# Kernel optimization log

Hardware: AMD Instinct MI355X
Metric: run time of the kernel (lower is better)

The kernel has to match this reference:

```python
import jax, jax.numpy as jnp
import numpy as np

B, T, M, P = 512, 64, 256, 256


def setup_inputs() -> dict:
    key = jax.random.key(0)
    ks = jax.random.split(key, 17)
    w = lambda i, shape: (jax.random.normal(ks[i], shape, jnp.float32) * 0.05)
    return {
        "encoded_inputs": jax.random.normal(ks[0], (B, T, M), jnp.float32),
        "y": jax.random.normal(ks[1], (B, T, 1), jnp.float32),
        "tar": jax.random.normal(ks[2], (B, 2), jnp.float32),
        "train": 1,
        "Wd_w": w(3, (M, 2 * P)), "Wd_b": w(4, (M,)),
        "Ud_w": w(5, (M, M)),
        "vd_w": w(6, (1, M)),
        "wt_w": w(7, (1, M + 1)), "wt_b": w(8, (1,)),
        "Wy_w": w(9, (P, P + M)), "Wy_b": w(10, (P,)),
        "vy_w": w(11, (1, P)), "vy_b": w(12, (1,)),
        "Wih": w(13, (4 * P, 1)), "Whh": w(14, (4 * P, P)),
        "bih": w(15, (4 * P,)), "bhh": w(16, (4 * P,)),
    }


def _lstm_cell(x, h, c, Wih, Whh, bih, bhh):
    # torch.nn.LSTMCell gate order: i, f, g, o
    g = x @ Wih.T + h @ Whh.T + (bih + bhh)
    i, f, gg, o = jnp.split(g, 4, axis=1)
    c = jax.nn.sigmoid(f) * c + jax.nn.sigmoid(i) * jnp.tanh(gg)
    h = jax.nn.sigmoid(o) * jnp.tanh(c)
    return h, c


def reference(encoded_inputs, y, tar, train,
              Wd_w, Wd_b, Ud_w, vd_w, wt_w, wt_b,
              Wy_w, Wy_b, vy_w, vy_b, Wih, Whh, bih, bhh):
    Bn = encoded_inputs.shape[0]
    Pn = Whh.shape[1]
    Mn = encoded_inputs.shape[2]
    h0 = jnp.zeros((Bn, Pn), encoded_inputs.dtype)
    c0 = jnp.zeros((Bn, Pn), encoded_inputs.dtype)
    ctx0 = jnp.zeros((Bn, Mn), encoded_inputs.dtype)
    # U_d(encoded_inputs) is loop-invariant
    y1 = jnp.einsum('btm,nm->btn', encoded_inputs, Ud_w)  # (B,T,M)

    def attend(h, s):
        x1 = jnp.concatenate([h, s], axis=1) @ Wd_w.T + Wd_b      # (B,M)
        z1 = jnp.tanh(x1[:, None, :] + y1)                        # (B,T,M)
        l = jnp.einsum('btm,m->bt', z1, vd_w[0])                  # (B,T)
        beta = jax.nn.softmax(l, axis=1)
        return jnp.einsum('bt,btm->bm', beta, encoded_inputs)     # (B,M)

    def step(carry, y_t):
        h, s, _ = carry
        c_t = attend(h, s)
        y_til = jnp.concatenate([c_t, y_t], axis=1) @ wt_w.T + wt_b  # (B,1)
        h, s = _lstm_cell(y_til, h, s, Wih, Whh, bih, bhh)
        return (h, s, c_t), None

    (h, s, c_t), _ = jax.lax.scan(step, (h0, c0, ctx0), jnp.swapaxes(y, 0, 1))

    def head(h):
        return (jnp.concatenate([h, c_t], axis=1) @ Wy_w.T + Wy_b) @ vy_w.T + vy_b

    def extra(h, s, inp):
        y_til = jnp.concatenate([c_t, inp], axis=1) @ wt_w.T + wt_b
        h, s = _lstm_cell(y_til, h, s, Wih, Whh, bih, bhh)
        return h, s, head(h)

    y_Tp1 = head(h)
    if train:
        h, s, y_Tp2 = extra(h, s, tar[:, 0:1])
        h, s, y_Tp3 = extra(h, s, tar[:, 1:2])
    else:
        h, s, y_Tp2 = extra(h, s, y_Tp1)
        h, s, y_Tp3 = extra(h, s, y_Tp2)
    return (y_Tp1, y_Tp2, y_Tp3)
```

## Files before the change

### kernel.cpp

```cpp
#include <hip/hip_runtime.h>


typedef unsigned short u16;
typedef unsigned int u32;
typedef _Float16 half_t;
typedef half_t h2 __attribute__((ext_vector_type(2)));

#define BB 512
#define TT 64
#define MM 256
#define PP 256
#define YS 264
#define ES 68

#define WD16_OFF  0
#define WHH16_OFF 131072
#define WY16_OFF  393216
#define WQ_ELEMS  524288
#define WQ_BYTES  (WQ_ELEMS * 2)

struct H8 { h2 p[4]; };

#if defined(__has_builtin)
#if __has_builtin(__builtin_amdgcn_fdot2)
#define FDOT2(a, b, c) __builtin_amdgcn_fdot2((a), (b), (c), false)
#endif
#endif
#ifndef FDOT2
__device__ __forceinline__ float FDOT2(h2 a, h2 b, float c) {
  return c + (float)a[0] * (float)b[0] + (float)a[1] * (float)b[1];
}
#endif

__device__ __forceinline__ float dot8(const H8 w, const H8 a, float acc) {
  acc = FDOT2(w.p[0], a.p[0], acc);
  acc = FDOT2(w.p[1], a.p[1], acc);
  acc = FDOT2(w.p[2], a.p[2], acc);
  acc = FDOT2(w.p[3], a.p[3], acc);
  return acc;
}
__device__ __forceinline__ u16 f2h(float f) {
  union { half_t h; u16 u; } x; x.h = (half_t)f; return x.u;
}
__device__ __forceinline__ void unpackH8(const H8 v, float f[8]) {
#pragma unroll
  for (int i = 0; i < 8; ++i) f[i] = (float)v.p[i >> 1][i & 1];
}
__device__ __forceinline__ void ldf8(const float* p, float f[8]) {
  float4 a = *(const float4*)p;
  float4 b = *(const float4*)(p + 4);
  f[0]=a.x; f[1]=a.y; f[2]=a.z; f[3]=a.w;
  f[4]=b.x; f[5]=b.y; f[6]=b.z; f[7]=b.w;
}
__device__ __forceinline__ float tanh_fast(float x) {
  float e = __builtin_amdgcn_exp2f(x * 2.885390081777927f);
  return 1.0f - 2.0f * __builtin_amdgcn_rcpf(1.0f + e);
}
__device__ __forceinline__ float sigmoid_fast(float x) {
  float e = __builtin_amdgcn_exp2f(x * -1.4426950408889634f);
  return __builtin_amdgcn_rcpf(1.0f + e);
}

__global__ __launch_bounds__(256) void prep_kernel(
    const float* __restrict__ Wd, const float* __restrict__ Whh,
    const float* __restrict__ Wy, u16* __restrict__ o) {
  int i = blockIdx.x * 256 + threadIdx.x;
  float v;
  if (i < WHH16_OFF) {
    int ki = i & 7, n = (i >> 3) & 255, kb = i >> 11;
    v = Wd[n * 512 + kb * 8 + ki];
  } else if (i < WY16_OFF) {
    int r = i - WHH16_OFF;
    int ki = r & 7, n = (r >> 3) & 1023, kb = r >> 13;
    v = Whh[n * 256 + kb * 8 + ki];
  } else {
    int r = i - WY16_OFF;
    int ki = r & 7, n = (r >> 3) & 255, kb = r >> 11;
    v = Wy[n * 512 + kb * 8 + ki];
  }
  o[i] = f2h(v);
}

template <int WQ>
__global__ __launch_bounds__(256, 2) void scan_kernel(
    const float* __restrict__ E,
    const float* __restrict__ yin,
    const float* __restrict__ tar,
    const int*   __restrict__ train,
    const void*  __restrict__ Wd_q,
    const float* __restrict__ Wd_b,
    const float* __restrict__ Ud_w,
    const float* __restrict__ vd_w,
    const float* __restrict__ wt_w,
    const float* __restrict__ wt_b,
    const void*  __restrict__ Wy_q,
    const float* __restrict__ Wy_b,
    const float* __restrict__ vy_w,
    const float* __restrict__ vy_b,
    const float* __restrict__ Wih,
    const void*  __restrict__ Whh_q,
    const float* __restrict__ bih,
    const float* __restrict__ bhh,
    float* __restrict__ out)
{
  __shared__ __align__(16) u16   y1l[TT * YS];
  __shared__ __align__(16) u16   e16T[MM * ES];
  __shared__ __align__(16) u32   hs16[256];
  __shared__ __align__(16) u32   ctx16p[128];
  __shared__ __align__(16) float ctx[MM];
  __shared__ __align__(16) float x1s[MM];
  __shared__ __align__(16) float lpart[4][TT];
  __shared__ __align__(16) u16   betas16[TT];
  __shared__ float red[4];
  __shared__ float sc[2];

  const int j = threadIdx.x;
  const int b = blockIdx.x;
  const int wv = j >> 6;

  hs16[j] = 0;
  float creg = 0.f;

  {
    const float* __restrict__ Eb = E + (size_t)b * TT * MM;
    for (int i = j; i < TT * MM; i += 256) {
      int t = i >> 8, m = i & 255;
      e16T[m * ES + t] = f2h(Eb[i]);
    }
  }

  {
    const float* __restrict__ Eb = E + (size_t)b * TT * MM;
    const float* __restrict__ Uj = Ud_w + (size_t)j * MM;
    for (int t0 = 0; t0 < TT; t0 += 16) {
      float acc[16];
#pragma unroll
      for (int i = 0; i < 16; ++i) acc[i] = 0.f;
      for (int m0 = 0; m0 < MM; m0 += 8) {
        float w[8]; ldf8(Uj + m0, w);
#pragma unroll
        for (int tt = 0; tt < 16; ++tt) {
          float e[8]; ldf8(Eb + (size_t)(t0 + tt) * MM + m0, e);
#pragma unroll
          for (int mm = 0; mm < 8; ++mm) acc[tt] = fmaf(e[mm], w[mm], acc[tt]);
        }
      }
#pragma unroll
      for (int tt = 0; tt < 16; ++tt)
        y1l[(t0 + tt) * YS + j] = f2h(acc[tt]);
    }
  }
  __syncthreads();

  auto mv4 = [&](float& g0, float& g1, float& g2, float& g3) {
    g0 = g1 = g2 = g3 = 0.f;
    if (WQ) {
      const u16* W = (const u16*)Whh_q;
      const u16* p0 = W + (size_t)j * 8;
      const u16* p1 = p0 + 256 * 8;
      const u16* p2 = p0 + 512 * 8;
      const u16* p3 = p0 + 768 * 8;
#pragma unroll 4
      for (int kb = 0; kb < 32; ++kb) {
        H8 hp = *(const H8*)&hs16[kb * 4];
        g0 = dot8(*(const H8*)p0, hp, g0); p0 += 8192;
        g1 = dot8(*(const H8*)p1, hp, g1); p1 += 8192;
        g2 = dot8(*(const H8*)p2, hp, g2); p2 += 8192;
        g3 = dot8(*(const H8*)p3, hp, g3); p3 += 8192;
      }
    } else {
      const float* W = (const float*)Whh_q;
      const float* p0 = W + (size_t)j * 256;
#pragma unroll 2
      for (int kb = 0; kb < 32; ++kb) {
        H8 hp = *(const H8*)&hs16[kb * 4];
        float hf[8]; unpackH8(hp, hf);
        float w0[8], w1[8], w2[8], w3[8];
        ldf8(p0 + kb * 8, w0);
        ldf8(p0 + 256 * 256 + kb * 8, w1);
        ldf8(p0 + 512 * 256 + kb * 8, w2);
        ldf8(p0 + 768 * 256 + kb * 8, w3);
#pragma unroll
        for (int i = 0; i < 8; ++i) {
          g0 = fmaf(hf[i], w0[i], g0);
          g1 = fmaf(hf[i], w1[i], g1);
          g2 = fmaf(hf[i], w2[i], g2);
          g3 = fmaf(hf[i], w3[i], g3);
        }
      }
    }
  };

  auto gates_apply = [&](float g0, float g1, float g2, float g3, float ytil) {
    g0 += ytil * Wih[j]       + bih[j]       + bhh[j];
    g1 += ytil * Wih[j + 256] + bih[j + 256] + bhh[j + 256];
    g2 += ytil * Wih[j + 512] + bih[j + 512] + bhh[j + 512];
    g3 += ytil * Wih[j + 768] + bih[j + 768] + bhh[j + 768];
    float c = sigmoid_fast(g1) * creg + sigmoid_fast(g0) * tanh_fast(g2);
    float h = sigmoid_fast(g3) * tanh_fast(c);
    creg = c;
    u16* hsu = (u16*)hs16;
    hsu[j] = f2h(h);
    hsu[256 + j] = f2h(c);
  };

  auto head_store = [&](int outIdx) {
    float p = 0.f;
    if (WQ) {
      const u16* W = (const u16*)Wy_q;
      const u16* ph = W + (size_t)j * 8;
      const u16* pc = W + (size_t)(32 * 256 + j) * 8;
#pragma unroll 4
      for (int kb = 0; kb < 32; ++kb) {
        H8 hp = *(const H8*)&hs16[kb * 4];
        H8 cp = *(const H8*)&ctx16p[kb * 4];
        p = dot8(*(const H8*)ph, hp, p); ph += 2048;
        p = dot8(*(const H8*)pc, cp, p); pc += 2048;
      }
    } else {
      const float* W = (const float*)Wy_q + (size_t)j * 512;
      for (int kb = 0; kb < 32; ++kb) {
        H8 hp = *(const H8*)&hs16[kb * 4];
        float hf[8]; unpackH8(hp, hf);
        float w0[8], w1[8];
        ldf8(W + kb * 8, w0);
        ldf8(W + 256 + kb * 8, w1);
#pragma unroll
        for (int i = 0; i < 8; ++i) {
          p = fmaf(hf[i], w0[i], p);
          p = fmaf(ctx[kb * 8 + i], w1[i], p);
        }
      }
    }
    float pp = (p + Wy_b[j]) * vy_w[j];
#pragma unroll
    for (int off = 32; off; off >>= 1) pp += __shfl_xor(pp, off, 64);
    if ((j & 63) == 0) red[wv] = pp;
    __syncthreads();
    if (j == 0) {
      float o = red[0] + red[1] + red[2] + red[3] + vy_b[0];
      out[(size_t)outIdx * BB + b] = o;
      sc[0] = o;
    }
    __syncthreads();
  };

  for (int step = 0; step < TT; ++step) {
    float ax0 = 0.f, ax1 = 0.f, g0, g1, g2, g3;
    {
      if (WQ) {
        const u16* Wd16 = (const u16*)Wd_q;
        const u16* Wh16 = (const u16*)Whh_q;
        const u16* pdh = Wd16 + (size_t)j * 8;
        const u16* pdc = Wd16 + (size_t)(32 * 256 + j) * 8;
        const u16* p0 = Wh16 + (size_t)j * 8;
        const u16* p1 = p0 + 256 * 8;
        const u16* p2 = p0 + 512 * 8;
        const u16* p3 = p0 + 768 * 8;
        float b0 = 0.f, b1 = 0.f, b2 = 0.f, b3 = 0.f;
#pragma unroll 4
        for (int kb = 0; kb < 32; ++kb) {
          H8 hp = *(const H8*)&hs16[kb * 4];
          H8 cp = *(const H8*)&hs16[128 + kb * 4];
          ax0 = dot8(*(const H8*)pdh, hp, ax0); pdh += 2048;
          ax1 = dot8(*(const H8*)pdc, cp, ax1); pdc += 2048;
          b0 = dot8(*(const H8*)p0, hp, b0); p0 += 8192;
          b1 = dot8(*(const H8*)p1, hp, b1); p1 += 8192;
          b2 = dot8(*(const H8*)p2, hp, b2); p2 += 8192;
          b3 = dot8(*(const H8*)p3, hp, b3); p3 += 8192;
        }
        g0 = b0; g1 = b1; g2 = b2; g3 = b3;
      } else {
        const float* wd = (const float*)Wd_q + (size_t)j * 512;
        const float* w0p = (const float*)Whh_q + (size_t)j * 256;
        float b0 = 0.f, b1 = 0.f, b2 = 0.f, b3 = 0.f;
#pragma unroll 2
        for (int kb = 0; kb < 32; ++kb) {
          H8 hp = *(const H8*)&hs16[kb * 4];
          H8 cp = *(const H8*)&hs16[128 + kb * 4];
          float hf[8], cf[8]; unpackH8(hp, hf); unpackH8(cp, cf);
          float wh[8], wc[8], w0[8], w1[8], w2[8], w3[8];
          ldf8(wd + kb * 8, wh);
          ldf8(wd + 256 + kb * 8, wc);
          ldf8(w0p + kb * 8, w0);
          ldf8(w0p + 256 * 256 + kb * 8, w1);
          ldf8(w0p + 512 * 256 + kb * 8, w2);
          ldf8(w0p + 768 * 256 + kb * 8, w3);
#pragma unroll
          for (int i = 0; i < 8; ++i) {
            ax0 = fmaf(hf[i], wh[i], ax0);
            ax1 = fmaf(cf[i], wc[i], ax1);
            b0 = fmaf(hf[i], w0[i], b0);
            b1 = fmaf(hf[i], w1[i], b1);
            b2 = fmaf(hf[i], w2[i], b2);
            b3 = fmaf(hf[i], w3[i], b3);
          }
        }
        g0 = b0; g1 = b1; g2 = b2; g3 = b3;
      }
      x1s[j] = ax0 + ax1 + Wd_b[j];
    }
    __syncthreads();

    {
      const int q = wv, tq = j & 63;
      const u16* __restrict__ yrow = &y1l[tq * YS + q * 64];
      const float* __restrict__ xp = &x1s[q * 64];
      const float* __restrict__ vp = vd_w + q * 64;
      float lp = 0.f;
#pragma unroll 2
      for (int m0 = 0; m0 < 64; m0 += 8) {
        H8 yv = *(const H8*)(yrow + m0);
        float yf[8]; unpackH8(yv, yf);
        float xf[8]; ldf8(xp + m0, xf);
        float vf[8]; ldf8(vp + m0, vf);
#pragma unroll
        for (int mm = 0; mm < 8; ++mm) {
          float z = tanh_fast(xf[mm] + yf[mm]);
          lp = fmaf(z, vf[mm], lp);
        }
      }
      lpart[q][tq] = lp;
    }
    __syncthreads();

    if (j < 64) {
      const int t = j;
      float l = lpart[0][t] + lpart[1][t] + lpart[2][t] + lpart[3][t];
      float mx = l;
#pragma unroll
      for (int off = 32; off; off >>= 1) mx = fmaxf(mx, __shfl_xor(mx, off, 64));
      float e = __builtin_amdgcn_exp2f((l - mx) * 1.4426950408889634f);
      float sm = e;
#pragma unroll
      for (int off = 32; off; off >>= 1) sm += __shfl_xor(sm, off, 64);
      betas16[t] = f2h(e * __builtin_amdgcn_rcpf(sm));
    }
    __syncthreads();

    {
      const u16* __restrict__ ep = &e16T[j * ES];
      float acc = 0.f;
#pragma unroll
      for (int t0 = 0; t0 < TT; t0 += 8) {
        h2 e0 = *(const h2*)(ep + t0);
        h2 e1 = *(const h2*)(ep + t0 + 2);
        h2 e2 = *(const h2*)(ep + t0 + 4);
        h2 e3 = *(const h2*)(ep + t0 + 6);
        H8 bp = *(const H8*)&betas16[t0];
        acc = FDOT2(bp.p[0], e0, acc);
        acc = FDOT2(bp.p[1], e1, acc);
        acc = FDOT2(bp.p[2], e2, acc);
        acc = FDOT2(bp.p[3], e3, acc);
      }
      ctx[j] = acc;
      ((u16*)ctx16p)[j] = f2h(acc);
    }
    {
      float p = ctx[j] * wt_w[j];
#pragma unroll
      for (int off = 32; off; off >>= 1) p += __shfl_xor(p, off, 64);
      if ((j & 63) == 0) red[wv] = p;
    }
    __syncthreads();
    {
      float ytil = red[0] + red[1] + red[2] + red[3]
                 + yin[(size_t)b * TT + step] * wt_w[MM] + wt_b[0];
      gates_apply(g0, g1, g2, g3, ytil);
    }
    __syncthreads();
  }

  float ctdot;
  {
    float p = ctx[j] * wt_w[j];
#pragma unroll
    for (int off = 32; off; off >>= 1) p += __shfl_xor(p, off, 64);
    if ((j & 63) == 0) red[wv] = p;
    __syncthreads();
    ctdot = red[0] + red[1] + red[2] + red[3];
    __syncthreads();
  }

  head_store(0);

  const int tr = train[0];
  for (int e = 0; e < 2; ++e) {
    float inp = tr ? tar[(size_t)b * 2 + e] : sc[0];
    float ytil = ctdot + inp * wt_w[MM] + wt_b[0];
    float g0, g1, g2, g3;
    mv4(g0, g1, g2, g3);
    gates_apply(g0, g1, g2, g3, ytil);
    __syncthreads();
    head_store(1 + e);
  }
}

extern "C" void kernel_launch(void* const* d_in, const int* in_sizes, int n_in,
                              void* d_out, int out_size, void* d_ws, size_t ws_size,
                              hipStream_t stream) {
  const float* E     = (const float*)d_in[0];
  const float* yin   = (const float*)d_in[1];
  const float* tar   = (const float*)d_in[2];
  const int*   train = (const int*)d_in[3];
  const float* Wd_w  = (const float*)d_in[4];
  const float* Wd_b  = (const float*)d_in[5];
  const float* Ud_w  = (const float*)d_in[6];
  const float* vd_w  = (const float*)d_in[7];
  const float* wt_w  = (const float*)d_in[8];
  const float* wt_b  = (const float*)d_in[9];
  const float* Wy_w  = (const float*)d_in[10];
  const float* Wy_b  = (const float*)d_in[11];
  const float* vy_w  = (const float*)d_in[12];
  const float* vy_b  = (const float*)d_in[13];
  const float* Wih   = (const float*)d_in[14];
  const float* Whh   = (const float*)d_in[15];
  const float* bih   = (const float*)d_in[16];
  const float* bhh   = (const float*)d_in[17];

  float* out = (float*)d_out;

  if (ws_size >= (size_t)WQ_BYTES) {
    u16* wq = (u16*)d_ws;
    prep_kernel<<<dim3(WQ_ELEMS / 256), dim3(256), 0, stream>>>(
        Wd_w, Whh, Wy_w, wq);
    scan_kernel<1><<<dim3(BB), dim3(256), 0, stream>>>(
        E, yin, tar, train, wq + WD16_OFF, Wd_b, Ud_w, vd_w, wt_w, wt_b,
        wq + WY16_OFF, Wy_b, vy_w, vy_b, Wih, wq + WHH16_OFF, bih, bhh, out);
  } else {
    scan_kernel<0><<<dim3(BB), dim3(256), 0, stream>>>(
        E, yin, tar, train, Wd_w, Wd_b, Ud_w, vd_w, wt_w, wt_b,
        Wy_w, Wy_b, vy_w, vy_b, Wih, Whh, bih, bhh, out);
  }

  (void)in_sizes; (void)n_in; (void)out_size;
}
```

Measured before the change: 1.189 ms.

## Process two batch rows per block to share weight loads across rows

Each 512-thread block now handles two batch elements. Every Whh/Wd/Wy weight row is loaded once and applied to both rows' hidden states, which roughly halves global weight traffic per batch element. The transposed LDS copy of E is removed: E is converted to fp16 in a separate prep kernel and the context sum reads it from global memory using beta values broadcast by shuffle. This adds extra barriers and cross-half partial-sum exchanges through LDS, doubles per-block LDS, and adds per-step global reads of E.

```diff
diff --git a/kernel.cpp b/kernel.cpp
--- a/kernel.cpp
+++ b/kernel.cpp
@@ -11,13 +11,15 @@
 #define MM 256
 #define PP 256
 #define YS 264
-#define ES 68
 
 #define WD16_OFF  0
 #define WHH16_OFF 131072
 #define WY16_OFF  393216
 #define WQ_ELEMS  524288
-#define WQ_BYTES  (WQ_ELEMS * 2)
+#define E16_OFF   524288
+#define E16_ELEMS (BB * TT * MM)
+#define WS_ELEMS  (WQ_ELEMS + E16_ELEMS)
+#define WS_BYTES  (WS_ELEMS * 2)
 
 struct H8 { h2 p[4]; };
 
@@ -61,7 +63,7 @@
   return __builtin_amdgcn_rcpf(1.0f + e);
 }
 
-__global__ __launch_bounds__(256) void prep_kernel(
+__global__ __launch_bounds__(256) void prep_w(
     const float* __restrict__ Wd, const float* __restrict__ Whh,
     const float* __restrict__ Wy, u16* __restrict__ o) {
   int i = blockIdx.x * 256 + threadIdx.x;
@@ -81,8 +83,14 @@
   o[i] = f2h(v);
 }
 
+__global__ __launch_bounds__(256) void prep_e(
+    const float* __restrict__ E, u16* __restrict__ o) {
+  int i = blockIdx.x * 256 + threadIdx.x;
+  o[E16_OFF + i] = f2h(E[i]);
+}
+
 template <int WQ>
-__global__ __launch_bounds__(256, 2) void scan_kernel(
+__global__ __launch_bounds__(512, 2) void scan_kernel(
     const float* __restrict__ E,
     const float* __restrict__ yin,
     const float* __restrict__ tar,
@@ -101,33 +109,29 @@
     const void*  __restrict__ Whh_q,
     const float* __restrict__ bih,
     const float* __restrict__ bhh,
+    const u16*   __restrict__ E16,
     float* __restrict__ out)
 {
-  __shared__ __align__(16) u16   y1l[TT * YS];
-  __shared__ __align__(16) u16   e16T[MM * ES];
-  __shared__ __align__(16) u32   hs16[256];
-  __shared__ __align__(16) u32   ctx16p[128];
-  __shared__ __align__(16) float ctx[MM];
-  __shared__ __align__(16) float x1s[MM];
-  __shared__ __align__(16) float lpart[4][TT];
-  __shared__ __align__(16) u16   betas16[TT];
-  __shared__ float red[4];
-  __shared__ float sc[2];
-
-  const int j = threadIdx.x;
-  const int b = blockIdx.x;
-  const int wv = j >> 6;
-
-  hs16[j] = 0;
+  __shared__ __align__(16) u16   y1l[2][TT * YS];
+  __shared__ __align__(16) u32   hs16[2 * 256];
+  __shared__ __align__(16) u32   ctx16p[2 * 128];
+  __shared__ __align__(16) float gbuf[2][1024];
+  __shared__ __align__(16) float part[2][2][256];
+  __shared__ __align__(16) float x1s[2][MM];
+  __shared__ __align__(16) float ctx[2][MM];
+  __shared__ __align__(16) float lpart[2][4][TT];
+  __shared__ float red[2][4];
+  __shared__ float sc_head[2];
+
+  const int tid  = threadIdx.x;
+  const int half = tid >> 8;
+  const int j    = tid & 255;
+  const int wv   = (tid >> 6) & 3;
+  const int lane = tid & 63;
+  const int b    = blockIdx.x * 2 + half;
+
+  hs16[tid] = 0;
   float creg = 0.f;
-
-  {
-    const float* __restrict__ Eb = E + (size_t)b * TT * MM;
-    for (int i = j; i < TT * MM; i += 256) {
-      int t = i >> 8, m = i & 255;
-      e16T[m * ES + t] = f2h(Eb[i]);
-    }
-  }
 
   {
     const float* __restrict__ Eb = E + (size_t)b * TT * MM;
@@ -147,166 +151,184 @@
       }
 #pragma unroll
       for (int tt = 0; tt < 16; ++tt)
-        y1l[(t0 + tt) * YS + j] = f2h(acc[tt]);
+        y1l[half][(t0 + tt) * YS + j] = f2h(acc[tt]);
     }
   }
   __syncthreads();
 
-  auto mv4 = [&](float& g0, float& g1, float& g2, float& g3) {
-    g0 = g1 = g2 = g3 = 0.f;
+  auto whh_mv = [&]() {
+    float b00 = 0.f, b01 = 0.f, b10 = 0.f, b11 = 0.f;
     if (WQ) {
-      const u16* W = (const u16*)Whh_q;
-      const u16* p0 = W + (size_t)j * 8;
-      const u16* p1 = p0 + 256 * 8;
-      const u16* p2 = p0 + 512 * 8;
-      const u16* p3 = p0 + 768 * 8;
+      const u16* p1 = (const u16*)Whh_q + (size_t)tid * 8;
+      const u16* p2 = p1 + 512 * 8;
 #pragma unroll 4
       for (int kb = 0; kb < 32; ++kb) {
-        H8 hp = *(const H8*)&hs16[kb * 4];
-        g0 = dot8(*(const H8*)p0, hp, g0); p0 += 8192;
-        g1 = dot8(*(const H8*)p1, hp, g1); p1 += 8192;
-        g2 = dot8(*(const H8*)p2, hp, g2); p2 += 8192;
-        g3 = dot8(*(const H8*)p3, hp, g3); p3 += 8192;
+        H8 h0 = *(const H8*)&hs16[kb * 4];
+        H8 h1 = *(const H8*)&hs16[256 + kb * 4];
+        H8 w1 = *(const H8*)p1; p1 += 8192;
+        H8 w2 = *(const H8*)p2; p2 += 8192;
+        b00 = dot8(w1, h0, b00);
+        b01 = dot8(w1, h1, b01);
+        b10 = dot8(w2, h0, b10);
+        b11 = dot8(w2, h1, b11);
       }
     } else {
-      const float* W = (const float*)Whh_q;
-      const float* p0 = W + (size_t)j * 256;
+      const float* q1 = (const float*)Whh_q + (size_t)tid * 256;
+      const float* q2 = q1 + 512 * 256;
 #pragma unroll 2
       for (int kb = 0; kb < 32; ++kb) {
-        H8 hp = *(const H8*)&hs16[kb * 4];
-        float hf[8]; unpackH8(hp, hf);
-        float w0[8], w1[8], w2[8], w3[8];
-        ldf8(p0 + kb * 8, w0);
-        ldf8(p0 + 256 * 256 + kb * 8, w1);
-        ldf8(p0 + 512 * 256 + kb * 8, w2);
-        ldf8(p0 + 768 * 256 + kb * 8, w3);
+        H8 h0 = *(const H8*)&hs16[kb * 4];
+        H8 h1 = *(const H8*)&hs16[256 + kb * 4];
+        float f0[8], f1[8]; unpackH8(h0, f0); unpackH8(h1, f1);
+        float w1[8], w2[8];
+        ldf8(q1 + kb * 8, w1);
+        ldf8(q2 + kb * 8, w2);
 #pragma unroll
         for (int i = 0; i < 8; ++i) {
-          g0 = fmaf(hf[i], w0[i], g0);
-          g1 = fmaf(hf[i], w1[i], g1);
-          g2 = fmaf(hf[i], w2[i], g2);
-          g3 = fmaf(hf[i], w3[i], g3);
-        }
-      }
-    }
+          b00 = fmaf(f0[i], w1[i], b00);
+          b01 = fmaf(f1[i], w1[i], b01);
+          b10 = fmaf(f0[i], w2[i], b10);
+          b11 = fmaf(f1[i], w2[i], b11);
+        }
+      }
+    }
+    gbuf[0][tid] = b00;       gbuf[1][tid] = b01;
+    gbuf[0][tid + 512] = b10; gbuf[1][tid + 512] = b11;
   };
 
-  auto gates_apply = [&](float g0, float g1, float g2, float g3, float ytil) {
-    g0 += ytil * Wih[j]       + bih[j]       + bhh[j];
-    g1 += ytil * Wih[j + 256] + bih[j + 256] + bhh[j + 256];
-    g2 += ytil * Wih[j + 512] + bih[j + 512] + bhh[j + 512];
-    g3 += ytil * Wih[j + 768] + bih[j + 768] + bhh[j + 768];
+  auto gates_apply = [&](float ytil) {
+    float g0 = gbuf[half][j]       + ytil * Wih[j]       + bih[j]       + bhh[j];
+    float g1 = gbuf[half][j + 256] + ytil * Wih[j + 256] + bih[j + 256] + bhh[j + 256];
+    float g2 = gbuf[half][j + 512] + ytil * Wih[j + 512] + bih[j + 512] + bhh[j + 512];
+    float g3 = gbuf[half][j + 768] + ytil * Wih[j + 768] + bih[j + 768] + bhh[j + 768];
     float c = sigmoid_fast(g1) * creg + sigmoid_fast(g0) * tanh_fast(g2);
     float h = sigmoid_fast(g3) * tanh_fast(c);
     creg = c;
     u16* hsu = (u16*)hs16;
-    hsu[j] = f2h(h);
-    hsu[256 + j] = f2h(c);
+    hsu[half * 512 + j]       = f2h(h);
+    hsu[half * 512 + 256 + j] = f2h(c);
   };
 
   auto head_store = [&](int outIdx) {
-    float p = 0.f;
+    float p0 = 0.f, p1 = 0.f;
     if (WQ) {
-      const u16* W = (const u16*)Wy_q;
-      const u16* ph = W + (size_t)j * 8;
-      const u16* pc = W + (size_t)(32 * 256 + j) * 8;
+      const u16* pw = (const u16*)Wy_q + (size_t)half * 32 * 2048 + (size_t)j * 8;
+      const u32* a0 = half ? &ctx16p[0] : &hs16[0];
+      const u32* a1 = half ? &ctx16p[128] : &hs16[256];
 #pragma unroll 4
       for (int kb = 0; kb < 32; ++kb) {
-        H8 hp = *(const H8*)&hs16[kb * 4];
-        H8 cp = *(const H8*)&ctx16p[kb * 4];
-        p = dot8(*(const H8*)ph, hp, p); ph += 2048;
-        p = dot8(*(const H8*)pc, cp, p); pc += 2048;
+        H8 w = *(const H8*)pw; pw += 2048;
+        p0 = dot8(w, *(const H8*)&a0[kb * 4], p0);
+        p1 = dot8(w, *(const H8*)&a1[kb * 4], p1);
       }
     } else {
-      const float* W = (const float*)Wy_q + (size_t)j * 512;
+      const float* pw = (const float*)Wy_q + (size_t)j * 512 + half * 256;
       for (int kb = 0; kb < 32; ++kb) {
-        H8 hp = *(const H8*)&hs16[kb * 4];
-        float hf[8]; unpackH8(hp, hf);
-        float w0[8], w1[8];
-        ldf8(W + kb * 8, w0);
-        ldf8(W + 256 + kb * 8, w1);
-#pragma unroll
-        for (int i = 0; i < 8; ++i) {
-          p = fmaf(hf[i], w0[i], p);
-          p = fmaf(ctx[kb * 8 + i], w1[i], p);
-        }
-      }
-    }
-    float pp = (p + Wy_b[j]) * vy_w[j];
-#pragma unroll
-    for (int off = 32; off; off >>= 1) pp += __shfl_xor(pp, off, 64);
-    if ((j & 63) == 0) red[wv] = pp;
+        float w[8]; ldf8(pw + kb * 8, w);
+        if (half) {
+#pragma unroll
+          for (int i = 0; i < 8; ++i) {
+            p0 = fmaf(ctx[0][kb * 8 + i], w[i], p0);
+            p1 = fmaf(ctx[1][kb * 8 + i], w[i], p1);
+          }
+        } else {
+          H8 h0 = *(const H8*)&hs16[kb * 4];
+          H8 h1 = *(const H8*)&hs16[256 + kb * 4];
+          float f0[8], f1[8]; unpackH8(h0, f0); unpackH8(h1, f1);
+#pragma unroll
+          for (int i = 0; i < 8; ++i) {
+            p0 = fmaf(f0[i], w[i], p0);
+            p1 = fmaf(f1[i], w[i], p1);
+          }
+        }
+      }
+    }
+    part[half][0][j] = p0;
+    part[half][1][j] = p1;
+    __syncthreads();
+    {
+      float hp = part[0][half][j] + part[1][half][j] + Wy_b[j];
+      float pp = hp * vy_w[j];
+#pragma unroll
+      for (int off = 32; off; off >>= 1) pp += __shfl_xor(pp, off, 64);
+      if (lane == 0) red[half][wv] = pp;
+    }
     __syncthreads();
     if (j == 0) {
-      float o = red[0] + red[1] + red[2] + red[3] + vy_b[0];
+      float o = red[half][0] + red[half][1] + red[half][2] + red[half][3]
+              + vy_b[0];
       out[(size_t)outIdx * BB + b] = o;
-      sc[0] = o;
+      sc_head[half] = o;
     }
     __syncthreads();
   };
 
   for (int step = 0; step < TT; ++step) {
-    float ax0 = 0.f, ax1 = 0.f, g0, g1, g2, g3;
     {
+      float ax0 = 0.f, ax1 = 0.f;
+      float b00 = 0.f, b01 = 0.f, b10 = 0.f, b11 = 0.f;
       if (WQ) {
-        const u16* Wd16 = (const u16*)Wd_q;
-        const u16* Wh16 = (const u16*)Whh_q;
-        const u16* pdh = Wd16 + (size_t)j * 8;
-        const u16* pdc = Wd16 + (size_t)(32 * 256 + j) * 8;
-        const u16* p0 = Wh16 + (size_t)j * 8;
-        const u16* p1 = p0 + 256 * 8;
-        const u16* p2 = p0 + 512 * 8;
-        const u16* p3 = p0 + 768 * 8;
-        float b0 = 0.f, b1 = 0.f, b2 = 0.f, b3 = 0.f;
+        const u16* pd = (const u16*)Wd_q + (size_t)half * 32 * 2048 + (size_t)j * 8;
+        const u16* p1 = (const u16*)Whh_q + (size_t)tid * 8;
+        const u16* p2 = p1 + 512 * 8;
+        const int ao = half * 128;
 #pragma unroll 4
         for (int kb = 0; kb < 32; ++kb) {
-          H8 hp = *(const H8*)&hs16[kb * 4];
-          H8 cp = *(const H8*)&hs16[128 + kb * 4];
-          ax0 = dot8(*(const H8*)pdh, hp, ax0); pdh += 2048;
-          ax1 = dot8(*(const H8*)pdc, cp, ax1); pdc += 2048;
-          b0 = dot8(*(const H8*)p0, hp, b0); p0 += 8192;
-          b1 = dot8(*(const H8*)p1, hp, b1); p1 += 8192;
-          b2 = dot8(*(const H8*)p2, hp, b2); p2 += 8192;
-          b3 = dot8(*(const H8*)p3, hp, b3); p3 += 8192;
-        }
-        g0 = b0; g1 = b1; g2 = b2; g3 = b3;
+          H8 h0 = *(const H8*)&hs16[kb * 4];
+          H8 h1 = *(const H8*)&hs16[256 + kb * 4];
+          H8 a0 = *(const H8*)&hs16[ao + kb * 4];
+          H8 a1 = *(const H8*)&hs16[256 + ao + kb * 4];
+          H8 wd = *(const H8*)pd; pd += 2048;
+          H8 w1 = *(const H8*)p1; p1 += 8192;
+          H8 w2 = *(const H8*)p2; p2 += 8192;
+          ax0 = dot8(wd, a0, ax0);
+          ax1 = dot8(wd, a1, ax1);
+          b00 = dot8(w1, h0, b00);
+          b01 = dot8(w1, h1, b01);
+          b10 = dot8(w2, h0, b10);
+          b11 = dot8(w2, h1, b11);
+        }
       } else {
-        const float* wd = (const float*)Wd_q + (size_t)j * 512;
-        const float* w0p = (const float*)Whh_q + (size_t)j * 256;
-        float b0 = 0.f, b1 = 0.f, b2 = 0.f, b3 = 0.f;
+        const float* pd = (const float*)Wd_q + (size_t)j * 512 + half * 256;
+        const float* q1 = (const float*)Whh_q + (size_t)tid * 256;
+        const float* q2 = q1 + 512 * 256;
+        const int ao = half * 128;
 #pragma unroll 2
         for (int kb = 0; kb < 32; ++kb) {
-          H8 hp = *(const H8*)&hs16[kb * 4];
-          H8 cp = *(const H8*)&hs16[128 + kb * 4];
-          float hf[8], cf[8]; unpackH8(hp, hf); unpackH8(cp, cf);
-          float wh[8], wc[8], w0[8], w1[8], w2[8], w3[8];
-          ldf8(wd + kb * 8, wh);
-          ldf8(wd + 256 + kb * 8, wc);
-          ldf8(w0p + kb * 8, w0);
-          ldf8(w0p + 256 * 256 + kb * 8, w1);
-          ldf8(w0p + 512 * 256 + kb * 8, w2);
-          ldf8(w0p + 768 * 256 + kb * 8, w3);
+          H8 h0 = *(const H8*)&hs16[kb * 4];
+          H8 h1 = *(const H8*)&hs16[256 + kb * 4];
+          H8 c0 = *(const H8*)&hs16[ao + kb * 4];
+          H8 c1 = *(const H8*)&hs16[256 + ao + kb * 4];
+          float f0[8], f1[8], e0[8], e1[8];
+          unpackH8(h0, f0); unpackH8(h1, f1); unpackH8(c0, e0); unpackH8(c1, e1);
+          float wd[8], w1[8], w2[8];
+          ldf8(pd + kb * 8, wd);
+          ldf8(q1 + kb * 8, w1);
+          ldf8(q2 + kb * 8, w2);
 #pragma unroll
           for (int i = 0; i < 8; ++i) {
-            ax0 = fmaf(hf[i], wh[i], ax0);
-            ax1 = fmaf(cf[i], wc[i], ax1);
-            b0 = fmaf(hf[i], w0[i], b0);
-            b1 = fmaf(hf[i], w1[i], b1);
-            b2 = fmaf(hf[i], w2[i], b2);
-            b3 = fmaf(hf[i], w3[i], b3);
+            ax0 = fmaf(e0[i], wd[i], ax0);
+            ax1 = fmaf(e1[i], wd[i], ax1);
+            b00 = fmaf(f0[i], w1[i], b00);
+            b01 = fmaf(f1[i], w1[i], b01);
+            b10 = fmaf(f0[i], w2[i], b10);
+            b11 = fmaf(f1[i], w2[i], b11);
           }
         }
-        g0 = b0; g1 = b1; g2 = b2; g3 = b3;
-      }
-      x1s[j] = ax0 + ax1 + Wd_b[j];
-    }
+      }
+      part[half][0][j] = ax0;
+      part[half][1][j] = ax1;
+      gbuf[0][tid] = b00;       gbuf[1][tid] = b01;
+      gbuf[0][tid + 512] = b10; gbuf[1][tid + 512] = b11;
+    }
+    __syncthreads();
+    x1s[half][j] = part[0][half][j] + part[1][half][j] + Wd_b[j];
     __syncthreads();
 
     {
-      const int q = wv, tq = j & 63;
-      const u16* __restrict__ yrow = &y1l[tq * YS + q * 64];
-      const float* __restrict__ xp = &x1s[q * 64];
-      const float* __restrict__ vp = vd_w + q * 64;
+      const u16* __restrict__ yrow = &y1l[half][lane * YS + wv * 64];
+      const float* __restrict__ xp = &x1s[half][wv * 64];
+      const float* __restrict__ vp = vd_w + wv * 64;
       float lp = 0.f;
 #pragma unroll 2
       for (int m0 = 0; m0 < 64; m0 += 8) {
@@ -320,13 +342,14 @@
           lp = fmaf(z, vf[mm], lp);
         }
       }
-      lpart[q][tq] = lp;
-    }
-    __syncthreads();
-
-    if (j < 64) {
-      const int t = j;
-      float l = lpart[0][t] + lpart[1][t] + lpart[2][t] + lpart[3][t];
+      lpart[half][wv][lane] = lp;
+    }
+    __syncthreads();
+
+    float ctv;
+    {
+      float l = lpart[half][0][lane] + lpart[half][1][lane]
+              + lpart[half][2][lane] + lpart[half][3][lane];
       float mx = l;
 #pragma unroll
       for (int off = 32; off; off >>= 1) mx = fmaxf(mx, __shfl_xor(mx, off, 64));
@@ -334,63 +357,62 @@
       float sm = e;
 #pragma unroll
       for (int off = 32; off; off >>= 1) sm += __shfl_xor(sm, off, 64);
-      betas16[t] = f2h(e * __builtin_amdgcn_rcpf(sm));
+      float beta = e * __builtin_amdgcn_rcpf(sm);
+
+      float acc = 0.f;
+      if (WQ) {
+        const half_t* __restrict__ ep = (const half_t*)E16 + (size_t)b * TT * MM + j;
+#pragma unroll 8
+        for (int t = 0; t < TT; ++t) {
+          float bt = __shfl(beta, t, 64);
+          acc = fmaf(bt, (float)ep[(size_t)t * MM], acc);
+        }
+      } else {
+        const float* __restrict__ ep = E + (size_t)b * TT * MM + j;
+#pragma unroll 8
+        for (int t = 0; t < TT; ++t) {
+          float bt = __shfl(beta, t, 64);
+          acc = fmaf(bt, ep[(size_t)t * MM], acc);
+        }
+      }
+      ctv = acc;
+      ctx[half][j] = acc;
+      ((u16*)ctx16p)[half * 256 + j] = f2h(acc);
+
+      float p = ctv * wt_w[j];
+#pragma unroll
+      for (int off = 32; off; off >>= 1) p += __shfl_xor(p, off, 64);
+      if (lane == 0) red[half][wv] = p;
     }
     __syncthreads();
 
     {
-      const u16* __restrict__ ep = &e16T[j * ES];
-      float acc = 0.f;
-#pragma unroll
-      for (int t0 = 0; t0 < TT; t0 += 8) {
-        h2 e0 = *(const h2*)(ep + t0);
-        h2 e1 = *(const h2*)(ep + t0 + 2);
-        h2 e2 = *(const h2*)(ep + t0 + 4);
-        h2 e3 = *(const h2*)(ep + t0 + 6);
-        H8 bp = *(const H8*)&betas16[t0];
-        acc = FDOT2(bp.p[0], e0, acc);
-        acc = FDOT2(bp.p[1], e1, acc);
-        acc = FDOT2(bp.p[2], e2, acc);
-        acc = FDOT2(bp.p[3], e3, acc);
-      }
-      ctx[j] = acc;
-      ((u16*)ctx16p)[j] = f2h(acc);
-    }
-    {
-      float p = ctx[j] * wt_w[j];
-#pragma unroll
-      for (int off = 32; off; off >>= 1) p += __shfl_xor(p, off, 64);
-      if ((j & 63) == 0) red[wv] = p;
-    }
-    __syncthreads();
-    {
-      float ytil = red[0] + red[1] + red[2] + red[3]
+      float ytil = red[half][0] + red[half][1] + red[half][2] + red[half][3]
                  + yin[(size_t)b * TT + step] * wt_w[MM] + wt_b[0];
-      gates_apply(g0, g1, g2, g3, ytil);
+      gates_apply(ytil);
     }
     __syncthreads();
   }
 
   float ctdot;
   {
-    float p = ctx[j] * wt_w[j];
+    float p = ctx[half][j] * wt_w[j];
 #pragma unroll
     for (int off = 32; off; off >>= 1) p += __shfl_xor(p, off, 64);
-    if ((j & 63) == 0) red[wv] = p;
-    __syncthreads();
-    ctdot = red[0] + red[1] + red[2] + red[3];
-    __syncthreads();
+    if (lane == 0) red[half][wv] = p;
+    __syncthreads();
+    ctdot = red[half][0] + red[half][1] + red[half][2] + red[half][3];
   }
 
   head_store(0);
 
   const int tr = train[0];
   for (int e = 0; e < 2; ++e) {
-    float inp = tr ? tar[(size_t)b * 2 + e] : sc[0];
+    float inp = tr ? tar[(size_t)b * 2 + e] : sc_head[half];
     float ytil = ctdot + inp * wt_w[MM] + wt_b[0];
-    float g0, g1, g2, g3;
-    mv4(g0, g1, g2, g3);
-    gates_apply(g0, g1, g2, g3, ytil);
+    whh_mv();
+    __syncthreads();
+    gates_apply(ytil);
     __syncthreads();
     head_store(1 + e);
   }
@@ -420,17 +442,18 @@
 
   float* out = (float*)d_out;
 
-  if (ws_size >= (size_t)WQ_BYTES) {
+  if (ws_size >= (size_t)WS_BYTES) {
     u16* wq = (u16*)d_ws;
-    prep_kernel<<<dim3(WQ_ELEMS / 256), dim3(256), 0, stream>>>(
-        Wd_w, Whh, Wy_w, wq);
-    scan_kernel<1><<<dim3(BB), dim3(256), 0, stream>>>(
+    prep_w<<<dim3(WQ_ELEMS / 256), dim3(256), 0, stream>>>(Wd_w, Whh, Wy_w, wq);
+    prep_e<<<dim3(E16_ELEMS / 256), dim3(256), 0, stream>>>(E, wq);
+    scan_kernel<1><<<dim3(BB / 2), dim3(512), 0, stream>>>(
         E, yin, tar, train, wq + WD16_OFF, Wd_b, Ud_w, vd_w, wt_w, wt_b,
-        wq + WY16_OFF, Wy_b, vy_w, vy_b, Wih, wq + WHH16_OFF, bih, bhh, out);
+        wq + WY16_OFF, Wy_b, vy_w, vy_b, Wih, wq + WHH16_OFF, bih, bhh,
+        wq + E16_OFF, out);
   } else {
-    scan_kernel<0><<<dim3(BB), dim3(256), 0, stream>>>(
+    scan_kernel<0><<<dim3(BB / 2), dim3(512), 0, stream>>>(
         E, yin, tar, train, Wd_w, Wd_b, Ud_w, vd_w, wt_w, wt_b,
-        Wy_w, Wy_b, vy_w, vy_b, Wih, Whh, bih, bhh, out);
+        Wy_w, Wy_b, vy_w, vy_b, Wih, Whh, bih, bhh, (const u16*)nullptr, out);
   }
 
   (void)in_sizes; (void)n_in; (void)out_size;
```

Result: no change. 1.195 ms (+0.5%).

## Compute softmax and context per wavefront redundantly to eliminate block barriers

Applied to the files above, without the earlier changes.

Each wavefront now computes the full softmax over time and the full context vector itself, using a private copy of the attention weights. The wt dot product is reduced within a wave, so the cross-wave reduction is gone. The barrier after the x1 write is dropped because each wave reads only the x1 entries it wrote. Together these cut the block-wide synchronisations per timestep from five to two. In exchange, the context computation is repeated four times, once per wave.

```diff
diff --git a/kernel.cpp b/kernel.cpp
--- a/kernel.cpp
+++ b/kernel.cpp
@@ -17,7 +17,7 @@
 #define WHH16_OFF 131072
 #define WY16_OFF  393216
 #define WQ_ELEMS  524288
-#define WQ_BYTES  (WQ_ELEMS * 2)
+#define WQ_BYTES  ((size_t)WQ_ELEMS * 2)
 
 struct H8 { h2 p[4]; };
 
@@ -61,7 +61,7 @@
   return __builtin_amdgcn_rcpf(1.0f + e);
 }
 
-__global__ __launch_bounds__(256) void prep_kernel(
+__global__ __launch_bounds__(256) void prep_w(
     const float* __restrict__ Wd, const float* __restrict__ Whh,
     const float* __restrict__ Wy, u16* __restrict__ o) {
   int i = blockIdx.x * 256 + threadIdx.x;
@@ -110,13 +110,14 @@
   __shared__ __align__(16) float ctx[MM];
   __shared__ __align__(16) float x1s[MM];
   __shared__ __align__(16) float lpart[4][TT];
-  __shared__ __align__(16) u16   betas16[TT];
-  __shared__ float red[4];
-  __shared__ float sc[2];
-
-  const int j = threadIdx.x;
-  const int b = blockIdx.x;
-  const int wv = j >> 6;
+  __shared__ __align__(16) u16   betas_w[4 * TT];
+  __shared__ float red[4], red2[4];
+  __shared__ float sc_head[1];
+
+  const int j    = threadIdx.x;
+  const int b    = blockIdx.x;
+  const int wv   = j >> 6;
+  const int lane = j & 63;
 
   hs16[j] = 0;
   float creg = 0.f;
@@ -152,11 +153,10 @@
   }
   __syncthreads();
 
-  auto mv4 = [&](float& g0, float& g1, float& g2, float& g3) {
+  auto whh_mv = [&](float& g0, float& g1, float& g2, float& g3) {
     g0 = g1 = g2 = g3 = 0.f;
     if (WQ) {
-      const u16* W = (const u16*)Whh_q;
-      const u16* p0 = W + (size_t)j * 8;
+      const u16* p0 = (const u16*)Whh_q + (size_t)j * 8;
       const u16* p1 = p0 + 256 * 8;
       const u16* p2 = p0 + 512 * 8;
       const u16* p3 = p0 + 768 * 8;
@@ -169,8 +169,7 @@
         g3 = dot8(*(const H8*)p3, hp, g3); p3 += 8192;
       }
     } else {
-      const float* W = (const float*)Whh_q;
-      const float* p0 = W + (size_t)j * 256;
+      const float* p0 = (const float*)Whh_q + (size_t)j * 256;
 #pragma unroll 2
       for (int kb = 0; kb < 32; ++kb) {
         H8 hp = *(const H8*)&hs16[kb * 4];
@@ -200,16 +199,15 @@
     float h = sigmoid_fast(g3) * tanh_fast(c);
     creg = c;
     u16* hsu = (u16*)hs16;
-    hsu[j] = f2h(h);
+    hsu[j]       = f2h(h);
     hsu[256 + j] = f2h(c);
   };
 
   auto head_store = [&](int outIdx) {
     float p = 0.f;
     if (WQ) {
-      const u16* W = (const u16*)Wy_q;
-      const u16* ph = W + (size_t)j * 8;
-      const u16* pc = W + (size_t)(32 * 256 + j) * 8;
+      const u16* ph = (const u16*)Wy_q + (size_t)j * 8;
+      const u16* pc = (const u16*)Wy_q + (size_t)(32 * 256 + j) * 8;
 #pragma unroll 4
       for (int kb = 0; kb < 32; ++kb) {
         H8 hp = *(const H8*)&hs16[kb * 4];
@@ -235,25 +233,24 @@
     float pp = (p + Wy_b[j]) * vy_w[j];
 #pragma unroll
     for (int off = 32; off; off >>= 1) pp += __shfl_xor(pp, off, 64);
-    if ((j & 63) == 0) red[wv] = pp;
+    if (lane == 0) red[wv] = pp;
     __syncthreads();
     if (j == 0) {
       float o = red[0] + red[1] + red[2] + red[3] + vy_b[0];
       out[(size_t)outIdx * BB + b] = o;
-      sc[0] = o;
+      sc_head[0] = o;
     }
     __syncthreads();
   };
 
   for (int step = 0; step < TT; ++step) {
-    float ax0 = 0.f, ax1 = 0.f, g0, g1, g2, g3;
+    float g0, g1, g2, g3;
     {
+      float ax0 = 0.f, ax1 = 0.f;
       if (WQ) {
-        const u16* Wd16 = (const u16*)Wd_q;
-        const u16* Wh16 = (const u16*)Whh_q;
-        const u16* pdh = Wd16 + (size_t)j * 8;
-        const u16* pdc = Wd16 + (size_t)(32 * 256 + j) * 8;
-        const u16* p0 = Wh16 + (size_t)j * 8;
+        const u16* pdh = (const u16*)Wd_q + (size_t)j * 8;
+        const u16* pdc = (const u16*)Wd_q + (size_t)(32 * 256 + j) * 8;
+        const u16* p0 = (const u16*)Whh_q + (size_t)j * 8;
         const u16* p1 = p0 + 256 * 8;
         const u16* p2 = p0 + 512 * 8;
         const u16* p3 = p0 + 768 * 8;
@@ -300,13 +297,11 @@
       }
       x1s[j] = ax0 + ax1 + Wd_b[j];
     }
-    __syncthreads();
 
     {
-      const int q = wv, tq = j & 63;
-      const u16* __restrict__ yrow = &y1l[tq * YS + q * 64];
-      const float* __restrict__ xp = &x1s[q * 64];
-      const float* __restrict__ vp = vd_w + q * 64;
+      const u16* __restrict__ yrow = &y1l[lane * YS + wv * 64];
+      const float* __restrict__ xp = &x1s[wv * 64];
+      const float* __restrict__ vp = vd_w + wv * 64;
       float lp = 0.f;
 #pragma unroll 2
       for (int m0 = 0; m0 < 64; m0 += 8) {
@@ -320,13 +315,13 @@
           lp = fmaf(z, vf[mm], lp);
         }
       }
-      lpart[q][tq] = lp;
-    }
-    __syncthreads();
-
-    if (j < 64) {
-      const int t = j;
-      float l = lpart[0][t] + lpart[1][t] + lpart[2][t] + lpart[3][t];
+      lpart[wv][lane] = lp;
+    }
+    __syncthreads();
+
+    {
+      float l = lpart[0][lane] + lpart[1][lane]
+              + lpart[2][lane] + lpart[3][lane];
       float mx = l;
 #pragma unroll
       for (int off = 32; off; off >>= 1) mx = fmaxf(mx, __shfl_xor(mx, off, 64));
@@ -334,38 +329,31 @@
       float sm = e;
 #pragma unroll
       for (int off = 32; off; off >>= 1) sm += __shfl_xor(sm, off, 64);
-      betas16[t] = f2h(e * __builtin_amdgcn_rcpf(sm));
-    }
-    __syncthreads();
-
-    {
-      const u16* __restrict__ ep = &e16T[j * ES];
-      float acc = 0.f;
-#pragma unroll
-      for (int t0 = 0; t0 < TT; t0 += 8) {
-        h2 e0 = *(const h2*)(ep + t0);
-        h2 e1 = *(const h2*)(ep + t0 + 2);
-        h2 e2 = *(const h2*)(ep + t0 + 4);
-        h2 e3 = *(const h2*)(ep + t0 + 6);
-        H8 bp = *(const H8*)&betas16[t0];
-        acc = FDOT2(bp.p[0], e0, acc);
-        acc = FDOT2(bp.p[1], e1, acc);
-        acc = FDOT2(bp.p[2], e2, acc);
-        acc = FDOT2(bp.p[3], e3, acc);
-      }
-      ctx[j] = acc;
-      ((u16*)ctx16p)[j] = f2h(acc);
-    }
-    {
-      float p = ctx[j] * wt_w[j];
+      float beta = e * __builtin_amdgcn_rcpf(sm);
+      betas_w[wv * 64 + lane] = f2h(beta);
+
+      float ct[4];
+#pragma unroll
+      for (int q = 0; q < 4; ++q) {
+        const u16* __restrict__ ep = &e16T[(q * 64 + lane) * ES];
+        float acc = 0.f;
+#pragma unroll
+        for (int t0 = 0; t0 < TT; t0 += 8) {
+          H8 bp = *(const H8*)&betas_w[wv * 64 + t0];
+          H8 ev = *(const H8*)(ep + t0);
+          acc = dot8(bp, ev, acc);
+        }
+        ct[q] = acc;
+      }
+      ctx[wv * 64 + lane] = ct[wv];
+      ((u16*)ctx16p)[wv * 64 + lane] = f2h(ct[wv]);
+
+      float p = ct[0] * wt_w[lane]       + ct[1] * wt_w[64 + lane]
+              + ct[2] * wt_w[128 + lane] + ct[3] * wt_w[192 + lane];
 #pragma unroll
       for (int off = 32; off; off >>= 1) p += __shfl_xor(p, off, 64);
-      if ((j & 63) == 0) red[wv] = p;
-    }
-    __syncthreads();
-    {
-      float ytil = red[0] + red[1] + red[2] + red[3]
-                 + yin[(size_t)b * TT + step] * wt_w[MM] + wt_b[0];
+      float ytil = p + yin[(size_t)b * TT + step] * wt_w[MM] + wt_b[0];
+
       gates_apply(g0, g1, g2, g3, ytil);
     }
     __syncthreads();
@@ -376,9 +364,9 @@
     float p = ctx[j] * wt_w[j];
 #pragma unroll
     for (int off = 32; off; off >>= 1) p += __shfl_xor(p, off, 64);
-    if ((j & 63) == 0) red[wv] = p;
-    __syncthreads();
-    ctdot = red[0] + red[1] + red[2] + red[3];
+    if (lane == 0) red2[wv] = p;
+    __syncthreads();
+    ctdot = red2[0] + red2[1] + red2[2] + red2[3];
     __syncthreads();
   }
 
@@ -386,10 +374,11 @@
 
   const int tr = train[0];
   for (int e = 0; e < 2; ++e) {
-    float inp = tr ? tar[(size_t)b * 2 + e] : sc[0];
+    float g0, g1, g2, g3;
+    whh_mv(g0, g1, g2, g3);
+    __syncthreads();
+    float inp = tr ? tar[(size_t)b * 2 + e] : sc_head[0];
     float ytil = ctdot + inp * wt_w[MM] + wt_b[0];
-    float g0, g1, g2, g3;
-    mv4(g0, g1, g2, g3);
     gates_apply(g0, g1, g2, g3, ytil);
     __syncthreads();
     head_store(1 + e);
@@ -420,10 +409,9 @@
 
   float* out = (float*)d_out;
 
-  if (ws_size >= (size_t)WQ_BYTES) {
+  if (ws_size >= WQ_BYTES) {
     u16* wq = (u16*)d_ws;
-    prep_kernel<<<dim3(WQ_ELEMS / 256), dim3(256), 0, stream>>>(
-        Wd_w, Whh, Wy_w, wq);
+    prep_w<<<dim3(WQ_ELEMS / 256), dim3(256), 0, stream>>>(Wd_w, Whh, Wy_w, wq);
     scan_kernel<1><<<dim3(BB), dim3(256), 0, stream>>>(
         E, yin, tar, train, wq + WD16_OFF, Wd_b, Ud_w, vd_w, wt_w, wt_b,
         wq + WY16_OFF, Wy_b, vy_w, vy_b, Wih, wq + WHH16_OFF, bih, bhh, out);
```

Result: no change. 1.200 ms (+0.9%).
